# Kernel tuning notes

Measured on AMD Instinct MI355X. Metric: run time of the kernel, lower is better.

## Reference

```python
import jax, jax.numpy as jnp
import numpy as np

N_NODES = 160000
N_EDGES = 2560000
N_GRAPHS = 1024
D = 32


def _gcn_layer(x, W, b, row, col, w):
    # PyG GCNConv with add_self_loops=True (loop weight 1) and symmetric norm.
    xw = x @ W                                   # [N, D]
    deg = jax.ops.segment_sum(w, col, num_segments=N_NODES) + 1.0  # self-loop
    dinv = jax.lax.rsqrt(deg)                    # deg >= 1 so finite
    norm = dinv[row] * w * dinv[col]             # [E]
    agg = jax.ops.segment_sum(norm[:, None] * xw[row], col, num_segments=N_NODES)
    agg = agg + xw * (1.0 / deg)[:, None]        # self-loop message: dinv[i]^2 = 1/deg[i]
    return agg + b


def setup_inputs() -> dict:
    key = jax.random.key(0)
    ks = jax.random.split(key, 20)
    s = 0.1
    inp = {
        "x": jax.random.normal(ks[0], (N_NODES, 1), jnp.float32),
        "edge_indices": jax.random.randint(ks[1], (2, N_EDGES), 0, N_NODES),
        "edge_weights": jax.random.uniform(ks[2], (N_EDGES,), jnp.float32),
        "batch": jnp.sort(jax.random.randint(ks[3], (N_NODES,), 0, N_GRAPHS)),
        # pre-MLP (2 layers)
        "W_pre0": s * jax.random.normal(ks[4], (1, D), jnp.float32),
        "b_pre0": jnp.zeros((D,), jnp.float32),
        "W_pre1": s * jax.random.normal(ks[5], (D, D), jnp.float32),
        "b_pre1": jnp.zeros((D,), jnp.float32),
        # 3 GCNConv layers
        "W_g0": s * jax.random.normal(ks[6], (D, D), jnp.float32),
        "b_g0": jnp.zeros((D,), jnp.float32),
        "W_g1": s * jax.random.normal(ks[7], (D, D), jnp.float32),
        "b_g1": jnp.zeros((D,), jnp.float32),
        "W_g2": s * jax.random.normal(ks[8], (D, D), jnp.float32),
        "b_g2": jnp.zeros((D,), jnp.float32),
        # post-MLP (2 layers, last -> 1 + sigmoid)
        "W_post0": s * jax.random.normal(ks[9], (D, D), jnp.float32),
        "b_post0": jnp.zeros((D,), jnp.float32),
        "W_post1": s * jax.random.normal(ks[10], (D, 1), jnp.float32),
        "b_post1": jnp.zeros((1,), jnp.float32),
    }
    return inp


def reference(x, edge_indices, edge_weights, batch,
              W_pre0, b_pre0, W_pre1, b_pre1,
              W_g0, b_g0, W_g1, b_g1, W_g2, b_g2,
              W_post0, b_post0, W_post1, b_post1):
    row, col = edge_indices[0], edge_indices[1]
    # pre-MLP: Linear + ReLU x2
    h = jax.nn.relu(x @ W_pre0 + b_pre0)
    h = jax.nn.relu(h @ W_pre1 + b_pre1)
    h = jax.nn.relu(_gcn_layer(h, W_g0, b_g0, row, col, edge_weights))
    h = jax.nn.relu(_gcn_layer(h, W_g1, b_g1, row, col, edge_weights))
    h = jax.nn.relu(_gcn_layer(h, W_g2, b_g2, row, col, edge_weights))
    # global mean pool over batch ids
    sums = jax.ops.segment_sum(h, batch, num_segments=N_GRAPHS)
    cnts = jax.ops.segment_sum(jnp.ones((N_NODES,), h.dtype), batch, num_segments=N_GRAPHS)
    g = sums / jnp.maximum(cnts, 1.0)[:, None]
    # post-MLP: Linear+ReLU (dropout inactive in eval), then Linear+Sigmoid
    g = jax.nn.relu(g @ W_post0 + b_post0)
    out = jax.nn.sigmoid(g @ W_post1 + b_post1)
    return out
```

## Files before the change

### kernel.cpp

```cpp
#include <hip/hip_runtime.h>
#include <math.h>

#define DIM 32
#define NB 625
#define CAP 5120
#define CHUNK 8192
#define BMAX 7424

typedef float floatx2 __attribute__((ext_vector_type(2)));

__device__ __forceinline__ unsigned pack4_fp8(float a, float b, float c, float d) {
    unsigned v = 0;
    v = __builtin_amdgcn_cvt_pk_fp8_f32(a, b, v, false);
    v = __builtin_amdgcn_cvt_pk_fp8_f32(c, d, v, true);
    return v;
}

__global__ void setup_kernel(const int* __restrict__ batch, int* __restrict__ gptr,
                             int* __restrict__ bcur, int N, int G) {
    int n = blockIdx.x * blockDim.x + threadIdx.x;
    if (n < NB) bcur[n] = n * CAP;
    if (n >= N) return;
    int b = batch[n];
    int bp = (n == 0) ? -1 : batch[n - 1];
    for (int g = bp + 1; g <= b; g++) gptr[g] = n;
    if (n == N - 1) {
        for (int g = b + 1; g <= G; g++) gptr[g] = N;
    }
}

__global__ __launch_bounds__(1024) void passA_kernel(
        const int* __restrict__ row, const int* __restrict__ col,
        const float* __restrict__ w, int* __restrict__ bcur,
        unsigned long long* __restrict__ stage, int E) {
    __shared__ unsigned long long lrec[CHUNK];
    __shared__ int hist[NB];
    __shared__ int excl[NB + 1];
    __shared__ int gbase[NB];
    __shared__ int sc[1024];
    int t = threadIdx.x;
    int base = blockIdx.x * CHUNK;
    int cnt = min(CHUNK, E - base);
    int creg[8];

    for (int j = t; j < NB; j += 1024) hist[j] = 0;
    __syncthreads();

#pragma unroll
    for (int i = 0; i < 8; i++) {
        int e = base + i * 1024 + t;
        creg[i] = (e < E) ? col[e] : -1;
        if (creg[i] >= 0) atomicAdd(&hist[creg[i] >> 8], 1);
    }
    __syncthreads();

    int v = (t < NB) ? hist[t] : 0;
    sc[t] = v;
    __syncthreads();
#pragma unroll
    for (int off = 1; off < 1024; off <<= 1) {
        int u = (t >= off) ? sc[t - off] : 0;
        __syncthreads();
        sc[t] += u;
        __syncthreads();
    }
    if (t < NB) {
        int ex = sc[t] - v;
        excl[t] = ex;
        hist[t] = ex;
        gbase[t] = v ? atomicAdd(&bcur[t], v) : 0;
    }
    if (t == 0) excl[NB] = cnt;
    __syncthreads();

#pragma unroll
    for (int i = 0; i < 8; i++) {
        int e = base + i * 1024 + t;
        int c = creg[i];
        if (c >= 0) {
            unsigned long long rec = ((unsigned long long)(unsigned)row[e] << 40)
                                   | ((unsigned long long)(unsigned)(c & 255) << 32)
                                   | (unsigned long long)__float_as_uint(w[e]);
            int pos = atomicAdd(&hist[c >> 8], 1);
            lrec[pos] = rec;
        }
    }
    __syncthreads();

    for (int i = t; i < cnt; i += 1024) {
        int lo = 0, hi = NB;
        while (hi - lo > 1) {
            int mid = (lo + hi) >> 1;
            if (excl[mid] <= i) lo = mid; else hi = mid;
        }
        int gpos = gbase[lo] + (i - excl[lo]);
        if (gpos < (lo + 1) * CAP) stage[gpos] = lrec[i];
    }
}

__global__ void passB1_kernel(const unsigned long long* __restrict__ stage,
                              const int* __restrict__ bcur,
                              int* __restrict__ ptr, int* __restrict__ bsum,
                              float* __restrict__ dinv) {
    __shared__ int icnt[256];
    __shared__ float fdeg[256];
    __shared__ int s[256];
    int b = blockIdx.x;
    int t = threadIdx.x;
    icnt[t] = 0;
    fdeg[t] = 0.0f;
    __syncthreads();
    int s0 = b * CAP;
    int m = min(bcur[b] - s0, CAP);
    for (int i = t; i < m; i += 256) {
        unsigned long long rec = stage[s0 + i];
        int cj = (int)((rec >> 32) & 255);
        float wf = __uint_as_float((unsigned)rec);
        atomicAdd(&icnt[cj], 1);
        atomicAdd(&fdeg[cj], wf);
    }
    __syncthreads();
    int c = b * 256 + t;
    int v = ((icnt[t] + 8) >> 3) << 3;
    dinv[c] = rsqrtf(fdeg[t] + 1.0f);
    s[t] = v;
    __syncthreads();
#pragma unroll
    for (int off = 1; off < 256; off <<= 1) {
        int u = (t >= off) ? s[t - off] : 0;
        __syncthreads();
        s[t] += u;
        __syncthreads();
    }
    ptr[c] = s[t] - v;
    if (t == 255) bsum[b] = s[255];
}

__global__ void passB2_kernel(const unsigned long long* __restrict__ stage,
                              const int* __restrict__ bcur, int* __restrict__ ptr,
                              const int* __restrict__ bsum,
                              const float* __restrict__ dinv,
                              unsigned* __restrict__ edat, int N) {
    __shared__ unsigned limg[BMAX];
    __shared__ int lcur[256];
    __shared__ int red[256];
    int b = blockIdx.x;
    int t = threadIdx.x;
    int c = b * 256 + t;
    int p = 0;
    for (int j = t; j < b; j += 256) p += bsum[j];
    red[t] = p;
    __syncthreads();
#pragma unroll
    for (int off = 128; off > 0; off >>= 1) {
        if (t < off) red[t] += red[t + off];
        __syncthreads();
    }
    int S = red[0];
    int bs = bsum[b];
    int pl = ptr[c];
    lcur[t] = pl + 1;
    for (int i = t; i < bs; i += 256) limg[i] = 0;
    __syncthreads();
    float di = dinv[c];
    float d2 = di * di;
    unsigned qs = min((unsigned)(d2 * 16384.0f + 0.5f), 16383u);
    limg[pl] = ((unsigned)c << 14) | qs;
    int s0 = b * CAP;
    int m = min(bcur[b] - s0, CAP);
    for (int i = t; i < m; i += 256) {
        unsigned long long rec = stage[s0 + i];
        int r = (int)(rec >> 40);
        int cj = (int)((rec >> 32) & 255);
        float wf = __uint_as_float((unsigned)rec);
        float nm = dinv[r] * wf * dinv[b * 256 + cj];
        unsigned q = (unsigned)(nm * 16384.0f + 0.5f);
        q = min(q, 16383u);
        int pos = atomicAdd(&lcur[cj], 1);
        limg[pos] = ((unsigned)r << 14) | q;
    }
    __syncthreads();
    for (int i = t; i < bs; i += 256) edat[S + i] = limg[i];
    ptr[c] = S + pl;
    if (b == gridDim.x - 1 && t == 255) ptr[N] = S + bs;
}

__global__ void pre_kernel(const float* __restrict__ x,
                           const float* __restrict__ W0, const float* __restrict__ b0,
                           const float* __restrict__ W1, const float* __restrict__ b1,
                           const float* __restrict__ Wg,
                           unsigned char* __restrict__ xw8, int N) {
    int n = blockIdx.x * blockDim.x + threadIdx.x;
    if (n >= N) return;
    float xv = x[n];
    float h0[DIM];
#pragma unroll
    for (int k = 0; k < DIM; k++) h0[k] = fmaxf(xv * W0[k] + b0[k], 0.0f);
    float h1[DIM];
#pragma unroll
    for (int d = 0; d < DIM; d++) h1[d] = b1[d];
#pragma unroll
    for (int k = 0; k < DIM; k++) {
        float hk = h0[k];
#pragma unroll
        for (int d = 0; d < DIM; d++) h1[d] += hk * W1[k * DIM + d];
    }
#pragma unroll
    for (int d = 0; d < DIM; d++) h1[d] = fmaxf(h1[d], 0.0f);
    float o[DIM];
#pragma unroll
    for (int d = 0; d < DIM; d++) o[d] = 0.0f;
#pragma unroll
    for (int k = 0; k < DIM; k++) {
        float hk = h1[k];
#pragma unroll
        for (int d = 0; d < DIM; d++) o[d] += hk * Wg[k * DIM + d];
    }
    unsigned u[8];
#pragma unroll
    for (int i = 0; i < 8; i++)
        u[i] = pack4_fp8(o[4 * i], o[4 * i + 1], o[4 * i + 2], o[4 * i + 3]);
    uint4* dst = (uint4*)(xw8 + (size_t)n * 32);
    dst[0] = make_uint4(u[0], u[1], u[2], u[3]);
    dst[1] = make_uint4(u[4], u[5], u[6], u[7]);
}

__device__ __forceinline__ void gather_body(
        const unsigned char* __restrict__ xin, const unsigned* __restrict__ edat,
        int e0, int e1, int slot, int sub, float acc[8]) {
    floatx2 a0 = {0, 0}, a1 = {0, 0}, a2 = {0, 0}, a3 = {0, 0};
    for (int base = e0; base < e1; base += 8) {
        unsigned rec0 = edat[base + slot];
        unsigned rec1 = edat[base + 4 + slot];
        int r0 = (int)(rec0 >> 14);
        int r1 = (int)(rec1 >> 14);
        float nm0 = (float)(rec0 & 16383u) * (1.0f / 16384.0f);
        float nm1 = (float)(rec1 & 16383u) * (1.0f / 16384.0f);
        uint2 u0 = *(const uint2*)(xin + (size_t)r0 * 32 + sub * 8);
        uint2 u1 = *(const uint2*)(xin + (size_t)r1 * 32 + sub * 8);
        floatx2 w0; w0.x = nm0; w0.y = nm0;
        floatx2 w1; w1.x = nm1; w1.y = nm1;
        a0 += w0 * __builtin_amdgcn_cvt_pk_f32_fp8(u0.x, false);
        a1 += w0 * __builtin_amdgcn_cvt_pk_f32_fp8(u0.x, true);
        a2 += w0 * __builtin_amdgcn_cvt_pk_f32_fp8(u0.y, false);
        a3 += w0 * __builtin_amdgcn_cvt_pk_f32_fp8(u0.y, true);
        a0 += w1 * __builtin_amdgcn_cvt_pk_f32_fp8(u1.x, false);
        a1 += w1 * __builtin_amdgcn_cvt_pk_f32_fp8(u1.x, true);
        a2 += w1 * __builtin_amdgcn_cvt_pk_f32_fp8(u1.y, false);
        a3 += w1 * __builtin_amdgcn_cvt_pk_f32_fp8(u1.y, true);
    }
    acc[0] = a0.x; acc[1] = a0.y; acc[2] = a1.x; acc[3] = a1.y;
    acc[4] = a2.x; acc[5] = a2.y; acc[6] = a3.x; acc[7] = a3.y;
#pragma unroll
    for (int s = 8; s >= 4; s >>= 1) {
#pragma unroll
        for (int i = 0; i < 8; i++) acc[i] += __shfl_xor(acc[i], s, 64);
    }
}

__global__ void gm_kernel(const unsigned char* __restrict__ xin,
                          const unsigned* __restrict__ edat,
                          const int* __restrict__ ptr,
                          const float* __restrict__ bgl,
                          const float* __restrict__ Wn,
                          unsigned char* __restrict__ xout, int N) {
    __shared__ float hs[16][33];
    __shared__ float wsm[1024];
    int t = threadIdx.x;
    for (int j = t; j < 1024; j += 256) wsm[j] = Wn[j];
    int wv = (blockIdx.x * blockDim.x + t) >> 6;
    int n0 = wv * 4;
    int lane = t & 63;
    int sg   = lane >> 4;
    int slot = (lane >> 2) & 3;
    int sub  = lane & 3;
    int n = n0 + sg;
    int e0 = ptr[n], e1 = ptr[n + 1];
    float acc[8];
    gather_body(xin, edat, e0, e1, slot, sub, acc);
    if (slot == 0) {
        int ln = (t >> 6) * 4 + sg;
#pragma unroll
        for (int i = 0; i < 8; i++)
            hs[ln][sub * 8 + i] = fmaxf(acc[i] + bgl[sub * 8 + i], 0.0f);
    }
    __syncthreads();
    int ln = t >> 4, dg = t & 15;
    const float* hrow = hs[ln];
    float o0 = 0.0f, o1 = 0.0f;
#pragma unroll
    for (int k = 0; k < DIM; k++) {
        float hk = hrow[k];
        o0 += hk * wsm[k * DIM + dg * 2];
        o1 += hk * wsm[k * DIM + dg * 2 + 1];
    }
    unsigned v = __builtin_amdgcn_cvt_pk_fp8_f32(o0, o1, 0, false);
    int nodeG = blockIdx.x * 16 + ln;
    *(unsigned short*)(xout + (size_t)nodeG * 32 + dg * 2) = (unsigned short)(v & 0xffff);
}

__global__ void gather_kernel(const unsigned char* __restrict__ xw8,
                              const unsigned* __restrict__ edat,
                              const int* __restrict__ ptr,
                              const float* __restrict__ bg,
                              float* __restrict__ agg, int N) {
    int wv = (blockIdx.x * blockDim.x + threadIdx.x) >> 6;
    int n0 = wv * 4;
    if (n0 >= N) return;
    int lane = threadIdx.x & 63;
    int sg   = lane >> 4;
    int slot = (lane >> 2) & 3;
    int sub  = lane & 3;
    int n = n0 + sg;
    int e0 = ptr[n], e1 = ptr[n + 1];
    float acc[8];
    gather_body(xw8, edat, e0, e1, slot, sub, acc);
    if (slot == 0) {
        float4 v0 = make_float4(acc[0] + bg[sub * 8 + 0], acc[1] + bg[sub * 8 + 1],
                                acc[2] + bg[sub * 8 + 2], acc[3] + bg[sub * 8 + 3]);
        float4 v1 = make_float4(acc[4] + bg[sub * 8 + 4], acc[5] + bg[sub * 8 + 5],
                                acc[6] + bg[sub * 8 + 6], acc[7] + bg[sub * 8 + 7]);
        float4* dst = (float4*)(agg + (size_t)n * DIM + sub * 8);
        dst[0] = v0;
        dst[1] = v1;
    }
}

__global__ void pool_post_kernel(const float* __restrict__ agg, const int* __restrict__ gptr,
                                 const float* __restrict__ W0, const float* __restrict__ b0,
                                 const float* __restrict__ W1, const float* __restrict__ b1,
                                 float* __restrict__ out) {
    __shared__ float red[8][DIM];
    __shared__ float gv[DIM];
    __shared__ float pr[DIM];
    int g = blockIdx.x;
    int s0 = gptr[g], s1 = gptr[g + 1];
    int slot = threadIdx.x >> 5, d = threadIdx.x & 31;
    float acc = 0.0f;
    for (int n = s0 + slot; n < s1; n += 8)
        acc += fmaxf(agg[(size_t)n * DIM + d], 0.0f);
    red[slot][d] = acc;
    __syncthreads();
    if (threadIdx.x < DIM) {
        float t = 0.0f;
#pragma unroll
        for (int i = 0; i < 8; i++) t += red[i][threadIdx.x];
        float c = fmaxf((float)(s1 - s0), 1.0f);
        gv[threadIdx.x] = t / c;
    }
    __syncthreads();
    if (threadIdx.x < DIM) {
        int j = threadIdx.x;
        float p = b0[j];
#pragma unroll
        for (int k = 0; k < DIM; k++) p += gv[k] * W0[k * DIM + j];
        pr[j] = fmaxf(p, 0.0f) * W1[j];
    }
    __syncthreads();
    if (threadIdx.x == 0) {
        float a = b1[0];
#pragma unroll
        for (int j = 0; j < DIM; j++) a += pr[j];
        out[g] = 1.0f / (1.0f + expf(-a));
    }
}

extern "C" void kernel_launch(void* const* d_in, const int* in_sizes, int n_in,
                              void* d_out, int out_size, void* d_ws, size_t ws_size,
                              hipStream_t stream) {
    const float* x   = (const float*)d_in[0];
    const int*   ei  = (const int*)d_in[1];
    const float* ew  = (const float*)d_in[2];
    const int*   bat = (const int*)d_in[3];
    const float* Wpre0 = (const float*)d_in[4];
    const float* bpre0 = (const float*)d_in[5];
    const float* Wpre1 = (const float*)d_in[6];
    const float* bpre1 = (const float*)d_in[7];
    const float* Wg[3]  = {(const float*)d_in[8],  (const float*)d_in[10], (const float*)d_in[12]};
    const float* bg[3]  = {(const float*)d_in[9],  (const float*)d_in[11], (const float*)d_in[13]};
    const float* Wpost0 = (const float*)d_in[14];
    const float* bpost0 = (const float*)d_in[15];
    const float* Wpost1 = (const float*)d_in[16];
    const float* bpost1 = (const float*)d_in[17];
    float* out = (float*)d_out;

    const int N = in_sizes[0];
    const int E = in_sizes[2];
    const int G = out_size;

    const int* row = ei;
    const int* col = ei + E;

    float* ws = (float*)d_ws;
    size_t nd = (size_t)N * DIM;
    float*          agg   = ws;
    unsigned char*  xw8a  = (unsigned char*)(agg + nd);
    unsigned long long* stage = (unsigned long long*)ws;
    float*          dinv  = ws + nd + nd / 4;
    int*            ptr   = (int*)(dinv + N);
    int*            bsum  = ptr + (N + 2);
    int*            gptr  = bsum + 626;
    int*            bcur  = gptr + 1026;
    unsigned*       edat  = (unsigned*)(bcur + 626);
    unsigned char*  xw8b  = (unsigned char*)(edat + E + 8 * (size_t)N);

    const int B = 256;

    setup_kernel<<<(N + B - 1) / B, B, 0, stream>>>(bat, gptr, bcur, N, G);
    int nChunksA = (E + CHUNK - 1) / CHUNK;
    passA_kernel<<<nChunksA, 1024, 0, stream>>>(row, col, ew, bcur, stage, E);
    passB1_kernel<<<NB, B, 0, stream>>>(stage, bcur, ptr, bsum, dinv);
    passB2_kernel<<<NB, B, 0, stream>>>(stage, bcur, ptr, bsum, dinv, edat, N);

    pre_kernel<<<(N + B - 1) / B, B, 0, stream>>>(
        x, Wpre0, bpre0, Wpre1, bpre1, Wg[0], xw8a, N);

    long long gThreads = (long long)(N / 4) * 64;
    int gBlocks = (int)((gThreads + B - 1) / B);
    int fBlocks = N / 16;

    gm_kernel<<<fBlocks, B, 0, stream>>>(xw8a, edat, ptr, bg[0], Wg[1], xw8b, N);
    gm_kernel<<<fBlocks, B, 0, stream>>>(xw8b, edat, ptr, bg[1], Wg[2], xw8a, N);
    gather_kernel<<<gBlocks, B, 0, stream>>>(xw8a, edat, ptr, bg[2], agg, N);

    pool_post_kernel<<<G, 256, 0, stream>>>(agg, gptr, Wpost0, bpost0, Wpost1, bpost1, out);
}
```

Measured before the change: 307.2 us.

## Split fp8 feature table into lo/hi halves and gather each half separately

The 32-byte fp8 node feature rows are stored as two separate 16-byte tables (low and high 16 dims). Each gather makes two passes over a node's edges, one per half, so the randomly accessed table in each pass is half the size and more likely to stay in L2. Lanes now cover 8 edge slots by 2 sub-chunks, with a 16-edge unrolled loop plus an 8-edge tail, and edge records use nontemporal loads. The cost is reading the edge list twice, a wider shuffle reduction, and extra workspace for four half tables.

```diff
diff --git a/kernel.cpp b/kernel.cpp
--- a/kernel.cpp
+++ b/kernel.cpp
@@ -189,7 +189,8 @@
                            const float* __restrict__ W0, const float* __restrict__ b0,
                            const float* __restrict__ W1, const float* __restrict__ b1,
                            const float* __restrict__ Wg,
-                           unsigned char* __restrict__ xw8, int N) {
+                           unsigned char* __restrict__ xlo, unsigned char* __restrict__ xhi,
+                           int N) {
     int n = blockIdx.x * blockDim.x + threadIdx.x;
     if (n >= N) return;
     float xv = x[n];
@@ -220,24 +221,24 @@
 #pragma unroll
     for (int i = 0; i < 8; i++)
         u[i] = pack4_fp8(o[4 * i], o[4 * i + 1], o[4 * i + 2], o[4 * i + 3]);
-    uint4* dst = (uint4*)(xw8 + (size_t)n * 32);
-    dst[0] = make_uint4(u[0], u[1], u[2], u[3]);
-    dst[1] = make_uint4(u[4], u[5], u[6], u[7]);
-}
-
-__device__ __forceinline__ void gather_body(
-        const unsigned char* __restrict__ xin, const unsigned* __restrict__ edat,
-        int e0, int e1, int slot, int sub, float acc[8]) {
+    *(uint4*)(xlo + (size_t)n * 16) = make_uint4(u[0], u[1], u[2], u[3]);
+    *(uint4*)(xhi + (size_t)n * 16) = make_uint4(u[4], u[5], u[6], u[7]);
+}
+
+__device__ __forceinline__ void gather_half(
+        const unsigned char* __restrict__ tab, const unsigned* __restrict__ edat,
+        int e0, int e1, int slot, int subL, float acc[8]) {
     floatx2 a0 = {0, 0}, a1 = {0, 0}, a2 = {0, 0}, a3 = {0, 0};
-    for (int base = e0; base < e1; base += 8) {
-        unsigned rec0 = edat[base + slot];
-        unsigned rec1 = edat[base + 4 + slot];
+    int base = e0;
+    for (; base + 16 <= e1; base += 16) {
+        unsigned rec0 = __builtin_nontemporal_load(&edat[base + slot]);
+        unsigned rec1 = __builtin_nontemporal_load(&edat[base + 8 + slot]);
         int r0 = (int)(rec0 >> 14);
         int r1 = (int)(rec1 >> 14);
         float nm0 = (float)(rec0 & 16383u) * (1.0f / 16384.0f);
         float nm1 = (float)(rec1 & 16383u) * (1.0f / 16384.0f);
-        uint2 u0 = *(const uint2*)(xin + (size_t)r0 * 32 + sub * 8);
-        uint2 u1 = *(const uint2*)(xin + (size_t)r1 * 32 + sub * 8);
+        uint2 u0 = *(const uint2*)(tab + (size_t)r0 * 16 + subL * 8);
+        uint2 u1 = *(const uint2*)(tab + (size_t)r1 * 16 + subL * 8);
         floatx2 w0; w0.x = nm0; w0.y = nm0;
         floatx2 w1; w1.x = nm1; w1.y = nm1;
         a0 += w0 * __builtin_amdgcn_cvt_pk_f32_fp8(u0.x, false);
@@ -249,21 +250,29 @@
         a2 += w1 * __builtin_amdgcn_cvt_pk_f32_fp8(u1.y, false);
         a3 += w1 * __builtin_amdgcn_cvt_pk_f32_fp8(u1.y, true);
     }
+    if (base < e1) {
+        unsigned rec0 = __builtin_nontemporal_load(&edat[base + slot]);
+        int r0 = (int)(rec0 >> 14);
+        float nm0 = (float)(rec0 & 16383u) * (1.0f / 16384.0f);
+        uint2 u0 = *(const uint2*)(tab + (size_t)r0 * 16 + subL * 8);
+        floatx2 w0; w0.x = nm0; w0.y = nm0;
+        a0 += w0 * __builtin_amdgcn_cvt_pk_f32_fp8(u0.x, false);
+        a1 += w0 * __builtin_amdgcn_cvt_pk_f32_fp8(u0.x, true);
+        a2 += w0 * __builtin_amdgcn_cvt_pk_f32_fp8(u0.y, false);
+        a3 += w0 * __builtin_amdgcn_cvt_pk_f32_fp8(u0.y, true);
+    }
     acc[0] = a0.x; acc[1] = a0.y; acc[2] = a1.x; acc[3] = a1.y;
     acc[4] = a2.x; acc[5] = a2.y; acc[6] = a3.x; acc[7] = a3.y;
-#pragma unroll
-    for (int s = 8; s >= 4; s >>= 1) {
-#pragma unroll
-        for (int i = 0; i < 8; i++) acc[i] += __shfl_xor(acc[i], s, 64);
-    }
-}
-
-__global__ void gm_kernel(const unsigned char* __restrict__ xin,
+}
+
+__global__ void gm_kernel(const unsigned char* __restrict__ xlo_in,
+                          const unsigned char* __restrict__ xhi_in,
                           const unsigned* __restrict__ edat,
                           const int* __restrict__ ptr,
                           const float* __restrict__ bgl,
                           const float* __restrict__ Wn,
-                          unsigned char* __restrict__ xout, int N) {
+                          unsigned char* __restrict__ xlo_out,
+                          unsigned char* __restrict__ xhi_out, int N) {
     __shared__ float hs[16][33];
     __shared__ float wsm[1024];
     int t = threadIdx.x;
@@ -272,17 +281,29 @@
     int n0 = wv * 4;
     int lane = t & 63;
     int sg   = lane >> 4;
-    int slot = (lane >> 2) & 3;
-    int sub  = lane & 3;
+    int slot = (lane >> 1) & 7;
+    int subL = lane & 1;
     int n = n0 + sg;
     int e0 = ptr[n], e1 = ptr[n + 1];
-    float acc[8];
-    gather_body(xin, edat, e0, e1, slot, sub, acc);
+    float alo[8], ahi[8];
+    gather_half(xlo_in, edat, e0, e1, slot, subL, alo);
+    gather_half(xhi_in, edat, e0, e1, slot, subL, ahi);
+#pragma unroll
+    for (int s = 8; s >= 2; s >>= 1) {
+#pragma unroll
+        for (int i = 0; i < 8; i++) {
+            alo[i] += __shfl_xor(alo[i], s, 64);
+            ahi[i] += __shfl_xor(ahi[i], s, 64);
+        }
+    }
     if (slot == 0) {
         int ln = (t >> 6) * 4 + sg;
-#pragma unroll
-        for (int i = 0; i < 8; i++)
-            hs[ln][sub * 8 + i] = fmaxf(acc[i] + bgl[sub * 8 + i], 0.0f);
+        int dbase = subL * 8;
+#pragma unroll
+        for (int i = 0; i < 8; i++) {
+            hs[ln][dbase + i]      = fmaxf(alo[i] + bgl[dbase + i], 0.0f);
+            hs[ln][16 + dbase + i] = fmaxf(ahi[i] + bgl[16 + dbase + i], 0.0f);
+        }
     }
     __syncthreads();
     int ln = t >> 4, dg = t & 15;
@@ -296,10 +317,14 @@
     }
     unsigned v = __builtin_amdgcn_cvt_pk_fp8_f32(o0, o1, 0, false);
     int nodeG = blockIdx.x * 16 + ln;
-    *(unsigned short*)(xout + (size_t)nodeG * 32 + dg * 2) = (unsigned short)(v & 0xffff);
-}
-
-__global__ void gather_kernel(const unsigned char* __restrict__ xw8,
+    if (dg < 8)
+        *(unsigned short*)(xlo_out + (size_t)nodeG * 16 + dg * 2) = (unsigned short)(v & 0xffff);
+    else
+        *(unsigned short*)(xhi_out + (size_t)nodeG * 16 + (dg - 8) * 2) = (unsigned short)(v & 0xffff);
+}
+
+__global__ void gather_kernel(const unsigned char* __restrict__ xlo,
+                              const unsigned char* __restrict__ xhi,
                               const unsigned* __restrict__ edat,
                               const int* __restrict__ ptr,
                               const float* __restrict__ bg,
@@ -309,20 +334,36 @@
     if (n0 >= N) return;
     int lane = threadIdx.x & 63;
     int sg   = lane >> 4;
-    int slot = (lane >> 2) & 3;
-    int sub  = lane & 3;
+    int slot = (lane >> 1) & 7;
+    int subL = lane & 1;
     int n = n0 + sg;
     int e0 = ptr[n], e1 = ptr[n + 1];
-    float acc[8];
-    gather_body(xw8, edat, e0, e1, slot, sub, acc);
+    float alo[8], ahi[8];
+    gather_half(xlo, edat, e0, e1, slot, subL, alo);
+    gather_half(xhi, edat, e0, e1, slot, subL, ahi);
+#pragma unroll
+    for (int s = 8; s >= 2; s >>= 1) {
+#pragma unroll
+        for (int i = 0; i < 8; i++) {
+            alo[i] += __shfl_xor(alo[i], s, 64);
+            ahi[i] += __shfl_xor(ahi[i], s, 64);
+        }
+    }
     if (slot == 0) {
-        float4 v0 = make_float4(acc[0] + bg[sub * 8 + 0], acc[1] + bg[sub * 8 + 1],
-                                acc[2] + bg[sub * 8 + 2], acc[3] + bg[sub * 8 + 3]);
-        float4 v1 = make_float4(acc[4] + bg[sub * 8 + 4], acc[5] + bg[sub * 8 + 5],
-                                acc[6] + bg[sub * 8 + 6], acc[7] + bg[sub * 8 + 7]);
-        float4* dst = (float4*)(agg + (size_t)n * DIM + sub * 8);
-        dst[0] = v0;
-        dst[1] = v1;
+        int dbase = subL * 8;
+        float* dst = agg + (size_t)n * DIM;
+        *(float4*)(dst + dbase) = make_float4(
+            alo[0] + bg[dbase + 0], alo[1] + bg[dbase + 1],
+            alo[2] + bg[dbase + 2], alo[3] + bg[dbase + 3]);
+        *(float4*)(dst + dbase + 4) = make_float4(
+            alo[4] + bg[dbase + 4], alo[5] + bg[dbase + 5],
+            alo[6] + bg[dbase + 6], alo[7] + bg[dbase + 7]);
+        *(float4*)(dst + 16 + dbase) = make_float4(
+            ahi[0] + bg[16 + dbase + 0], ahi[1] + bg[16 + dbase + 1],
+            ahi[2] + bg[16 + dbase + 2], ahi[3] + bg[16 + dbase + 3]);
+        *(float4*)(dst + 16 + dbase + 4) = make_float4(
+            ahi[4] + bg[16 + dbase + 4], ahi[5] + bg[16 + dbase + 5],
+            ahi[6] + bg[16 + dbase + 6], ahi[7] + bg[16 + dbase + 7]);
     }
 }
 
@@ -394,7 +435,6 @@
     float* ws = (float*)d_ws;
     size_t nd = (size_t)N * DIM;
     float*          agg   = ws;
-    unsigned char*  xw8a  = (unsigned char*)(agg + nd);
     unsigned long long* stage = (unsigned long long*)ws;
     float*          dinv  = ws + nd + nd / 4;
     int*            ptr   = (int*)(dinv + N);
@@ -402,7 +442,10 @@
     int*            gptr  = bsum + 626;
     int*            bcur  = gptr + 1026;
     unsigned*       edat  = (unsigned*)(bcur + 626);
-    unsigned char*  xw8b  = (unsigned char*)(edat + E + 8 * (size_t)N);
+    unsigned char*  xlo_a = (unsigned char*)(edat + E + 8 * (size_t)N);
+    unsigned char*  xhi_a = xlo_a + (size_t)N * 16;
+    unsigned char*  xlo_b = xhi_a + (size_t)N * 16;
+    unsigned char*  xhi_b = xlo_b + (size_t)N * 16;
 
     const int B = 256;
 
@@ -413,15 +456,15 @@
     passB2_kernel<<<NB, B, 0, stream>>>(stage, bcur, ptr, bsum, dinv, edat, N);
 
     pre_kernel<<<(N + B - 1) / B, B, 0, stream>>>(
-        x, Wpre0, bpre0, Wpre1, bpre1, Wg[0], xw8a, N);
+        x, Wpre0, bpre0, Wpre1, bpre1, Wg[0], xlo_a, xhi_a, N);
 
     long long gThreads = (long long)(N / 4) * 64;
     int gBlocks = (int)((gThreads + B - 1) / B);
     int fBlocks = N / 16;
 
-    gm_kernel<<<fBlocks, B, 0, stream>>>(xw8a, edat, ptr, bg[0], Wg[1], xw8b, N);
-    gm_kernel<<<fBlocks, B, 0, stream>>>(xw8b, edat, ptr, bg[1], Wg[2], xw8a, N);
-    gather_kernel<<<gBlocks, B, 0, stream>>>(xw8a, edat, ptr, bg[2], agg, N);
+    gm_kernel<<<fBlocks, B, 0, stream>>>(xlo_a, xhi_a, edat, ptr, bg[0], Wg[1], xlo_b, xhi_b, N);
+    gm_kernel<<<fBlocks, B, 0, stream>>>(xlo_b, xhi_b, edat, ptr, bg[1], Wg[2], xlo_a, xhi_a, N);
+    gather_kernel<<<gBlocks, B, 0, stream>>>(xlo_a, xhi_a, edat, ptr, bg[2], agg, N);
 
     pool_post_kernel<<<G, 256, 0, stream>>>(agg, gptr, Wpost0, bpost0, Wpost1, bpost1, out);
 }
```

Result: slower. 382.1 us (+24.4%).
